# Optimization experiments

Hardware: AMD Instinct MI355X
Metric: run time of the kernel (lower is better)

## Reference

```python
import jax, jax.numpy as jnp
import numpy as np

K = 20          # neighbors, hardcoded in module
SLOPE = 0.2     # LeakyReLU negative slope
EPS = 1e-5      # BatchNorm eps (eval mode, running_mean=0, running_var=1)


def _knn_idx(x, k):
    # x: (B, N, C) -> (B, N, k) indices of k nearest neighbors (includes self)
    xx = jnp.sum(x * x, axis=-1)                      # (B, N)
    inner = jnp.einsum('bnc,bmc->bnm', x, x)          # (B, N, N)
    neg_sqdist = 2.0 * inner - xx[:, :, None] - xx[:, None, :]
    _, idx = jax.lax.top_k(neg_sqdist, k)
    return idx


def _graph_feature(x, k):
    # x: (B, N, C) -> edge features (B, N, k, 2C) = [x_j - x_i, x_i]
    idx = _knn_idx(x, k)
    feat = jax.vmap(lambda xt, ix: xt[ix])(x, idx)    # (B, N, k, C)
    xc = jnp.broadcast_to(x[:, :, None, :], feat.shape)
    return jnp.concatenate([feat - xc, xc], axis=-1)


def _bn_lrelu(h, g, b):
    # eval-mode BN (mean=0, var=1) + LeakyReLU(0.2)
    h = h * (g / jnp.sqrt(1.0 + EPS)) + b
    return jnp.where(h >= 0, h, SLOPE * h)


def _edge_conv(x, W, g, b):
    # EdgeConv block: graph feature -> 1x1 conv -> BN -> LeakyReLU -> max over k
    e = _graph_feature(x, K)                          # (B, N, k, 2C)
    h = jnp.einsum('bnkc,oc->bnko', e, W)
    h = _bn_lrelu(h, g, b)
    return jnp.max(h, axis=2)                         # (B, N, O)


def reference(x, W1, g1, b1, W2, g2, b2, W3, g3, b3, W4, g4, b4, W5, g5, b5, Wemb):
    # x: (B, N, 3) point cloud
    x1 = _edge_conv(x, W1, g1, b1)    # (B, N, 64)
    x2 = _edge_conv(x1, W2, g2, b2)   # (B, N, 64)
    x3 = _edge_conv(x2, W3, g3, b3)   # (B, N, 128)
    x4 = _edge_conv(x3, W4, g4, b4)   # (B, N, 256)
    h = jnp.concatenate([x1, x2, x3, x4], axis=-1)    # (B, N, 512)
    h = jnp.einsum('bnc,oc->bno', h, W5)              # conv5 (1x1)
    h = _bn_lrelu(h, g5, b5)
    h = jnp.max(h, axis=1)                            # global max pool -> (B, 512)
    feat = h[:, None, :]                              # (B, 1, 512)
    embedding = h @ Wemb.T                            # (B, 256)
    return (feat, embedding)


def setup_inputs() -> dict:
    key = jax.random.key(0)
    ks = jax.random.split(key, 18)
    B, N = 8, 2048
    num_features = 256

    def w(k, o, i):
        return jax.random.normal(k, (o, i), dtype=jnp.float32) * (1.0 / np.sqrt(i))

    return {
        'x':  jax.random.normal(ks[0], (B, N, 3), dtype=jnp.float32),
        'W1': w(ks[1], 64, 6),
        'g1': jnp.ones((64,), jnp.float32),  'b1': jnp.zeros((64,), jnp.float32),
        'W2': w(ks[2], 64, 128),
        'g2': jnp.ones((64,), jnp.float32),  'b2': jnp.zeros((64,), jnp.float32),
        'W3': w(ks[3], 128, 128),
        'g3': jnp.ones((128,), jnp.float32), 'b3': jnp.zeros((128,), jnp.float32),
        'W4': w(ks[4], 256, 256),
        'g4': jnp.ones((256,), jnp.float32), 'b4': jnp.zeros((256,), jnp.float32),
        'W5': w(ks[5], 512, 512),
        'g5': jnp.ones((512,), jnp.float32), 'b5': jnp.zeros((512,), jnp.float32),
        'Wemb': w(ks[6], num_features, 512),
    }
```

## Files before the change

### kernel.cpp

```cpp
#include <hip/hip_runtime.h>
#include <hip/hip_bf16.h>

#define BB 8
#define NN 2048
#define KK 20
#define BN (BB*NN)
#define RSQ 0.99999500003749969f

constexpr size_t OFF_XX  = 0;
constexpr size_t OFF_X1  = OFF_XX  + BN;
constexpr size_t OFF_X2  = OFF_X1  + (size_t)BN*64;
constexpr size_t OFF_X3  = OFF_X2  + (size_t)BN*64;
constexpr size_t OFF_X4  = OFF_X3  + (size_t)BN*128;
constexpr size_t OFF_SC  = OFF_X4  + (size_t)BN*256;
constexpr size_t OFF_ID  = OFF_SC  + (size_t)BN*160;
constexpr size_t OFF_W5T = OFF_ID  + (size_t)BN*20;
constexpr size_t OFF_MX  = OFF_W5T + 512*512;
constexpr size_t OFF_MN  = OFF_MX  + BB*512;
constexpr size_t OFF_WT2 = OFF_MN  + BB*512;
constexpr size_t OFF_WT3 = OFF_WT2 + 8192;
constexpr size_t OFF_WT4 = OFF_WT3 + 16384;
constexpr size_t WS_END  = OFF_WT4 + 65536;
constexpr size_t OFF_BIG = WS_END;
constexpr size_t OFF_XCAT = OFF_BIG + (size_t)16*1024*1024;
constexpr size_t WS_BIG_END = OFF_BIG + (size_t)BB*NN*NN;
static_assert(OFF_ID - OFF_X3 >= (size_t)4096*2048, "fallback dual dist fits");
static_assert(OFF_XCAT + (size_t)BN*768 <= WS_BIG_END, "xcat h/m/l fits in dist region");

typedef unsigned short u16;
typedef __attribute__((ext_vector_type(8))) short short8;
typedef __attribute__((ext_vector_type(8))) unsigned short ushort8;
typedef __attribute__((ext_vector_type(4))) float f32x4;

__device__ inline unsigned encf(float f){ unsigned u=__float_as_uint(f); return (u&0x80000000u)? ~u : (u|0x80000000u); }
__device__ inline float decf(unsigned e){ unsigned u=(e&0x80000000u)? (e&0x7fffffffu) : ~e; return __uint_as_float(u); }
__device__ inline float lrelu(float h){ return h>=0.f ? h : 0.2f*h; }
__device__ inline u16 bf16rne(float x){
  unsigned u = __float_as_uint(x);
  return (u16)((u + 0x7FFFu + ((u>>16)&1u)) >> 16);
}
__device__ inline float bf16f(u16 h){ return __uint_as_float((unsigned)h<<16); }
__device__ inline void bf16split3(float v, u16& h, u16& m, u16& l){
  h = bf16rne(v);  float r1 = v  - bf16f(h);
  m = bf16rne(r1); float r2 = r1 - bf16f(m);
  l = bf16rne(r2);
}

__device__ inline float readlane_f(float v, int sl){
  return __int_as_float(__builtin_amdgcn_readlane(__float_as_int(v), sl));
}

#define INSERT_CAND(cv, ci) { \
  unsigned long long mge = __ballot((lv > cv) || (lv == cv && li < ci)); \
  int pos = __popcll(mge); \
  float upv = __shfl_up(lv, 1); \
  int   upi = __shfl_up(li, 1); \
  bool shift = (lane > pos) && (lane < KK); \
  lv = (lane == pos) ? cv : (shift ? upv : lv); \
  li = (lane == pos) ? ci : (shift ? upi : li); \
  theta = readlane_f(lv, KK-1); }

#define BITONIC64_DESC(v, vi) { \
  _Pragma("unroll") \
  for(int k=2; k<=64; k<<=1){ \
    _Pragma("unroll") \
    for(int j=k>>1; j>=1; j>>=1){ \
      float ov = __shfl_xor(v, j); \
      int   oi = __shfl_xor(vi, j); \
      int partner = lane ^ j; \
      bool keepFirst = (((lane & k) == 0)) == (lane < partner); \
      bool before = (v > ov) || (v == ov && vi < oi); \
      if(keepFirst != before){ v = ov; vi = oi; } \
    } \
  } }


__global__ void prep_k(const float* W5, const float* W2, const float* W3, const float* W4,
                       float* W5T, float* WT2, float* WT3, float* WT4,
                       u16* w5h, u16* w5m, u16* w5l,
                       unsigned* mx, unsigned* mn){
  int i = blockIdx.x*256 + threadIdx.x;
  { int o = i>>9, c = i&511; W5T[c*512+o] = W5[i]; }
  {
    int rg = i>>13, kt = (i>>9)&15, l = (i>>3)&63, j = i&7;
    int o = rg*16 + (l&15);
    int c = kt*32 + ((l>>4)<<3) + j;
    u16 h,m,lo; bf16split3(W5[(size_t)o*512 + c], h, m, lo);
    w5h[i]=h; w5m[i]=m; w5l[i]=lo; }
  if(i < 65536){ int c = i>>9, o = i&511;
    WT4[i] = (o<256) ? W4[(size_t)o*256 + c] : W4[(size_t)(o-256)*256 + 128 + c]; }
  if(i < 16384){ int c = i>>8, o = i&255;
    WT3[i] = (o<128) ? W3[(size_t)o*128 + c] : W3[(size_t)(o-128)*128 + 64 + c]; }
  if(i <  8192){ int c = i>>7, o = i&127;
    WT2[i] = (o<64) ? W2[(size_t)o*128 + c] : W2[(size_t)(o-64)*128 + 64 + c]; }
  if(i <  4096){ mx[i] = 0x007FFFFFu; mn[i] = 0xFF800000u; }
}

template<int C>
__launch_bounds__(256) __global__ void sqnorm_k(const float* X, float* xx){
  int i = blockIdx.x*256 + threadIdx.x;
  const float* r = X + (size_t)i*C;
  float s = 0.f;
  #pragma unroll
  for(int c=0;c<C;c++) s = fmaf(r[c], r[c], s);
  xx[i] = s;
}

template<int C>
__launch_bounds__(256) __global__ void split_k(const float* __restrict__ X,
    u16* __restrict__ xh, u16* __restrict__ xm, u16* __restrict__ xl){
  constexpr int KT = C/32;
  const size_t t = (size_t)blockIdx.x*256 + threadIdx.x;
  const int l = (int)(t & 63);
  const size_t tile = t >> 6;
  const int kt = (int)(tile & (KT-1));
  const size_t rgG = tile / KT;
  const size_t row = rgG*16 + (l & 15);
  const int k = kt*32 + ((l>>4)<<3);
  const float* p = X + row*C + k;
  float4 v0 = *(const float4*)p;
  float4 v1 = *(const float4*)(p+4);
  float vs[8] = {v0.x,v0.y,v0.z,v0.w,v1.x,v1.y,v1.z,v1.w};
  ushort8 H,M,L;
  #pragma unroll
  for(int j=0;j<8;j++){ u16 h,m,lo; bf16split3(vs[j],h,m,lo); H[j]=h; M[j]=m; L[j]=lo; }
  *(ushort8*)(xh + t*8) = H;
  *(ushort8*)(xm + t*8) = M;
  *(ushort8*)(xl + t*8) = L;
}

#define FMA_ROW(I) \
  acc[I][0]=fmaf(a,b0v,acc[I][0]); acc[I][1]=fmaf(a,b1v,acc[I][1]); \
  acc[I][2]=fmaf(a,b2v,acc[I][2]); acc[I][3]=fmaf(a,b3v,acc[I][3]); \
  acc[I][4]=fmaf(a,b4v,acc[I][4]); acc[I][5]=fmaf(a,b5v,acc[I][5]); \
  acc[I][6]=fmaf(a,b6v,acc[I][6]); acc[I][7]=fmaf(a,b7v,acc[I][7]);

template<int C>
__launch_bounds__(256) __global__ void gemm_dist_k(const float* __restrict__ X, const float* __restrict__ xx,
                                                   float* __restrict__ dist, int b0){
  constexpr int AST = 188;
  __shared__ __align__(16) float a_sh[16*AST];
  __shared__ __align__(16) float b_sh[16*AST];
  __shared__ float sxn[128], sxm[128];
  const int tid = threadIdx.x;
  const int b   = b0 + blockIdx.z;
  const int mtile = blockIdx.x*128;
  const int ntile = blockIdx.y*128;
  const int tn = tid & 15, tm = tid >> 4;
  const float* Xb  = X  + (size_t)b*NN*C;
  const float* xxb = xx + (size_t)b*NN;
  if(tid < 128) sxn[tid] = xxb[ntile + tid];
  else          sxm[tid-128] = xxb[mtile + tid-128];
  float acc[8][8];
  #pragma unroll
  for(int i=0;i<8;i++){
    #pragma unroll
    for(int j=0;j<8;j++) acc[i][j]=0.f;
  }
  for(int cc=0; cc<C; cc+=16){
    __syncthreads();
    #pragma unroll
    for(int s=0;s<2;s++){
      int ii = tid + 256*s; int r = ii>>2, q = ii&3;
      int pr = r + 4*(r>>3);
      float4 va = *(const float4*)&Xb[(size_t)(ntile + r)*C + cc + 4*q];
      a_sh[(4*q+0)*AST + pr]=va.x; a_sh[(4*q+1)*AST + pr]=va.y;
      a_sh[(4*q+2)*AST + pr]=va.z; a_sh[(4*q+3)*AST + pr]=va.w;
      float4 vb = *(const float4*)&Xb[(size_t)(mtile + r)*C + cc + 4*q];
      b_sh[(4*q+0)*AST + pr]=vb.x; b_sh[(4*q+1)*AST + pr]=vb.y;
      b_sh[(4*q+2)*AST + pr]=vb.z; b_sh[(4*q+3)*AST + pr]=vb.w;
    }
    __syncthreads();
    #pragma unroll
    for(int c=0;c<16;c++){
      float4 A0 = *(const float4*)&a_sh[c*AST + 12*tn];
      float4 A1 = *(const float4*)&a_sh[c*AST + 12*tn + 4];
      float4 B0 = *(const float4*)&b_sh[c*AST + 12*tm];
      float4 B1 = *(const float4*)&b_sh[c*AST + 12*tm + 4];
      float b0v=B0.x,b1v=B0.y,b2v=B0.z,b3v=B0.w,b4v=B1.x,b5v=B1.y,b6v=B1.z,b7v=B1.w;
      float a;
      a=A0.x; FMA_ROW(0)
      a=A0.y; FMA_ROW(1)
      a=A0.z; FMA_ROW(2)
      a=A0.w; FMA_ROW(3)
      a=A1.x; FMA_ROW(4)
      a=A1.y; FMA_ROW(5)
      a=A1.z; FMA_ROW(6)
      a=A1.w; FMA_ROW(7)
    }
  }
  float xnr[8], xmr[8];
  #pragma unroll
  for(int i=0;i<8;i++){ xnr[i]=sxn[tn*8+i]; xmr[i]=sxm[tm*8+i]; }
  const size_t rowb = (size_t)blockIdx.z*NN + ntile + tn*8;
  #pragma unroll
  for(int i=0;i<8;i++){
    float4 w0, w1;
    w0.x=(2.f*acc[i][0]-xnr[i])-xmr[0]; w0.y=(2.f*acc[i][1]-xnr[i])-xmr[1];
    w0.z=(2.f*acc[i][2]-xnr[i])-xmr[2]; w0.w=(2.f*acc[i][3]-xnr[i])-xmr[3];
    w1.x=(2.f*acc[i][4]-xnr[i])-xmr[4]; w1.y=(2.f*acc[i][5]-xnr[i])-xmr[5];
    w1.z=(2.f*acc[i][6]-xnr[i])-xmr[6]; w1.w=(2.f*acc[i][7]-xnr[i])-xmr[7];
    float* dp = dist + (rowb + i)*NN + mtile + tm*8;
    *(float4*)dp = w0;
    *(float4*)(dp+4) = w1;
  }
}

template<int C>
__launch_bounds__(256) __global__ void mfma_dist_k(const u16* __restrict__ xh, const u16* __restrict__ xm,
    const u16* __restrict__ xl, const float* __restrict__ xx, float* __restrict__ dist){
  constexpr int KT = C/32;
  const int tid = threadIdx.x;
  const int l  = tid & 63, wv = tid >> 6;
  const int lg = l >> 4, lr = l & 15;
  const int b  = blockIdx.z;
  const int qrow0 = blockIdx.y*128 + (wv>>1)*64;
  const int crow0 = blockIdx.x*128 + (wv&1)*64;
  const size_t brg = (size_t)b*(NN/16);
  f32x4 acc[4][4];
  #pragma unroll
  for(int m=0;m<4;m++){
    #pragma unroll
    for(int n=0;n<4;n++) acc[m][n] = (f32x4){0.f,0.f,0.f,0.f};
  }
  const size_t abase = (brg + (qrow0>>4))*KT*512 + (size_t)l*8;
  const size_t bbase = (brg + (crow0>>4))*KT*512 + (size_t)l*8;
  for(int kt=0; kt<KT; kt++){
    short8 Ah[4], Am[4], Al[4], Bh[4], Bm[4], Bl[4];
    #pragma unroll
    for(int m=0;m<4;m++){
      size_t o = abase + (size_t)(m*KT + kt)*512;
      Ah[m] = *(const short8*)(xh + o);
      Am[m] = *(const short8*)(xm + o);
      Al[m] = *(const short8*)(xl + o);
    }
    #pragma unroll
    for(int n=0;n<4;n++){
      size_t o = bbase + (size_t)(n*KT + kt)*512;
      Bh[n] = *(const short8*)(xh + o);
      Bm[n] = *(const short8*)(xm + o);
      Bl[n] = *(const short8*)(xl + o);
    }
    #pragma unroll
    for(int m=0;m<4;m++){
      #pragma unroll
      for(int n=0;n<4;n++){
        acc[m][n] = __builtin_amdgcn_mfma_f32_16x16x32_bf16(Ah[m], Bh[n], acc[m][n], 0, 0, 0);
        acc[m][n] = __builtin_amdgcn_mfma_f32_16x16x32_bf16(Ah[m], Bm[n], acc[m][n], 0, 0, 0);
        acc[m][n] = __builtin_amdgcn_mfma_f32_16x16x32_bf16(Am[m], Bh[n], acc[m][n], 0, 0, 0);
        acc[m][n] = __builtin_amdgcn_mfma_f32_16x16x32_bf16(Ah[m], Bl[n], acc[m][n], 0, 0, 0);
        acc[m][n] = __builtin_amdgcn_mfma_f32_16x16x32_bf16(Al[m], Bh[n], acc[m][n], 0, 0, 0);
        acc[m][n] = __builtin_amdgcn_mfma_f32_16x16x32_bf16(Am[m], Bm[n], acc[m][n], 0, 0, 0);
      }
    }
  }
  const float* xxb = xx + (size_t)b*NN;
  float xxc[4];
  #pragma unroll
  for(int n=0;n<4;n++) xxc[n] = xxb[crow0 + n*16 + lr];
  #pragma unroll
  for(int m=0;m<4;m++){
    #pragma unroll
    for(int r=0;r<4;r++){
      int qr = qrow0 + m*16 + 4*lg + r;
      float xq = xxb[qr];
      float* dp = dist + ((size_t)b*NN + qr)*NN + crow0;
      #pragma unroll
      for(int n=0;n<4;n++) dp[n*16 + lr] = (2.f*acc[m][n][r] - xq) - xxc[n];
    }
  }
}

__launch_bounds__(256) __global__ void sel_k(const float* __restrict__ dist, int* __restrict__ id,
                                             int b0, int nrows){
  const int w = (blockIdx.x*256 + threadIdx.x) >> 6;
  const int lane = threadIdx.x & 63;
  if(w >= nrows) return;
  const float* dr = dist + (size_t)w*NN;
  float4 c0 = *(const float4*)&dr[4*lane];
  float cd0[4] = {c0.x, c0.y, c0.z, c0.w};
  int jbest = 0; float v = cd0[0];
  #pragma unroll
  for(int j=1;j<4;j++){ if(cd0[j] > v){ v = cd0[j]; jbest = j; } }
  int vi = 4*lane + jbest;
  BITONIC64_DESC(v, vi)
  float lv = (lane < KK) ? v : -INFINITY;
  int   li = (lane < KK) ? vi : 0;
  float theta = readlane_f(lv, KK-1);
  #pragma unroll
  for(int j=0;j<4;j++){
    float cand = (j == jbest) ? -INFINITY : cd0[j];
    unsigned long long bal = __ballot(cand > theta);
    while(bal){
      int bpos = __ffsll((unsigned long long)bal) - 1;
      bal &= bal - 1;
      float cv = readlane_f(cand, bpos);
      if(cv > theta){
        int ci = 4*bpos + j;
        INSERT_CAND(cv, ci)
      }
    }
  }
  for(int ms=256; ms<NN; ms+=256){
    float4 c4 = *(const float4*)&dr[ms + 4*lane];
    #pragma unroll
    for(int j=0;j<4;j++){
      float cand = (j==0)?c4.x:(j==1)?c4.y:(j==2)?c4.z:c4.w;
      unsigned long long bal = __ballot(cand > theta);
      while(bal){
        int bpos = __ffsll((unsigned long long)bal) - 1;
        bal &= bal - 1;
        float cv = readlane_f(cand, bpos);
        if(cv > theta){
          int ci = ms + 4*bpos + j;
          INSERT_CAND(cv, ci)
        }
      }
    }
  }
  if(lane < KK) id[((size_t)b0*NN + w)*KK + lane] = li;
}

__launch_bounds__(256) __global__ void sel3_k(const float* __restrict__ X, int* __restrict__ id){
  const int gw = (blockIdx.x*256 + threadIdx.x) >> 6;
  const int lane = threadIdx.x & 63;
  const int b = gw >> 11, n = gw & 2047;
  const float* Xb  = X + (size_t)b*NN*3;
  const float x0v = Xb[n*3], x1v = Xb[n*3+1], x2v = Xb[n*3+2];
  float xxn = 0.f;
  xxn = fmaf(x0v, x0v, xxn); xxn = fmaf(x1v, x1v, xxn); xxn = fmaf(x2v, x2v, xxn);
  float lv, theta; int li;
  {
    const float* p = Xb + (size_t)(4*lane)*3;
    float4 va = *(const float4*)p;
    float4 vb = *(const float4*)(p+4);
    float4 vc = *(const float4*)(p+8);
    float cx[4] = {va.x, va.w, vb.z, vc.y};
    float cy[4] = {va.y, vb.x, vb.w, vc.z};
    float cz[4] = {va.z, vb.y, vc.x, vc.w};
    float cd[4];
    #pragma unroll
    for(int j=0;j<4;j++){
      float s = 0.f;
      s = fmaf(x0v, cx[j], s); s = fmaf(x1v, cy[j], s); s = fmaf(x2v, cz[j], s);
      float xxm = 0.f;
      xxm = fmaf(cx[j], cx[j], xxm); xxm = fmaf(cy[j], cy[j], xxm); xxm = fmaf(cz[j], cz[j], xxm);
      cd[j] = (2.f*s - xxn) - xxm;
    }
    int jbest = 0; float v = cd[0];
    #pragma unroll
    for(int j=1;j<4;j++){ if(cd[j] > v){ v = cd[j]; jbest = j; } }
    int vi = 4*lane + jbest;
    BITONIC64_DESC(v, vi)
    lv = (lane < KK) ? v : -INFINITY;
    li = (lane < KK) ? vi : 0;
    theta = readlane_f(lv, KK-1);
    #pragma unroll
    for(int j=0;j<4;j++){
      float cand = (j == jbest) ? -INFINITY : cd[j];
      unsigned long long bal = __ballot(cand > theta);
      while(bal){
        int bpos = __ffsll((unsigned long long)bal) - 1;
        bal &= bal - 1;
        float cv = readlane_f(cand, bpos);
        if(cv > theta){
          int ci = 4*bpos + j;
          INSERT_CAND(cv, ci)
        }
      }
    }
  }
  for(int ms=256; ms<NN; ms+=256){
    const float* p = Xb + (size_t)(ms + 4*lane)*3;
    float4 va = *(const float4*)p;
    float4 vb = *(const float4*)(p+4);
    float4 vc = *(const float4*)(p+8);
    float cx[4] = {va.x, va.w, vb.z, vc.y};
    float cy[4] = {va.y, vb.x, vb.w, vc.z};
    float cz[4] = {va.z, vb.y, vc.x, vc.w};
    float cd[4];
    #pragma unroll
    for(int j=0;j<4;j++){
      float s = 0.f;
      s = fmaf(x0v, cx[j], s); s = fmaf(x1v, cy[j], s); s = fmaf(x2v, cz[j], s);
      float xxm = 0.f;
      xxm = fmaf(cx[j], cx[j], xxm); xxm = fmaf(cy[j], cy[j], xxm); xxm = fmaf(cz[j], cz[j], xxm);
      cd[j] = (2.f*s - xxn) - xxm;
    }
    #pragma unroll
    for(int j=0;j<4;j++){
      float cand = cd[j];
      unsigned long long bal = __ballot(cand > theta);
      while(bal){
        int bpos = __ffsll((unsigned long long)bal) - 1;
        bal &= bal - 1;
        float cv = readlane_f(cand, bpos);
        if(cv > theta){
          int ci = ms + 4*bpos + j;
          INSERT_CAND(cv, ci)
        }
      }
    }
  }
  if(lane < KK) id[(size_t)gw*KK + lane] = li;
}

__launch_bounds__(256) __global__ void qp3_k(const float* X, const float* W, float* qp){
  const int t   = blockIdx.x*256 + threadIdx.x;
  const int row = t >> 3;
  const int c0  = (t & 7) * 8;
  float xn[3];
  #pragma unroll
  for(int c=0;c<3;c++) xn[c] = X[(size_t)row*3 + c];
  for(int oi=c0; oi<c0+8; oi++){
    const float* w = W + (size_t)oi*6;
    float aq=0.f, ap=0.f;
    #pragma unroll
    for(int c=0;c<3;c++){ aq = fmaf(xn[c], w[c], aq); ap = fmaf(xn[c], w[3+c], ap); }
    qp[(size_t)row*128 + oi]      = aq;
    qp[(size_t)row*128 + 64 + oi] = ap;
  }
}

template<int CIN, int W2C>
__launch_bounds__(256) __global__ void qp_gemm_k(const float* __restrict__ X, const float* __restrict__ WT,
                                                 float* __restrict__ qp){
  constexpr int ASTA = 92;
  constexpr int ASTB = 188;
  __shared__ __align__(16) float a_sh[16*ASTA];
  __shared__ __align__(16) float b_sh[16*ASTB];
  const int tid = threadIdx.x;
  const int otile = blockIdx.x*128;
  const int rtile = blockIdx.y*64;
  const int tn = tid & 15, tm = tid >> 4;
  const int aoff = 4*tn + 4*(tn>>1);
  float acc[4][8];
  #pragma unroll
  for(int i=0;i<4;i++){
    #pragma unroll
    for(int j=0;j<8;j++) acc[i][j]=0.f;
  }
  for(int cc=0; cc<CIN; cc+=16){
    __syncthreads();
    { int r = tid>>2, q = tid&3;
      int pr = r + 4*(r>>3);
      float4 va = *(const float4*)&X[(size_t)(rtile + r)*CIN + cc + 4*q];
      a_sh[(4*q+0)*ASTA + pr]=va.x; a_sh[(4*q+1)*ASTA + pr]=va.y;
      a_sh[(4*q+2)*ASTA + pr]=va.z; a_sh[(4*q+3)*ASTA + pr]=va.w; }
    #pragma unroll
    for(int s=0;s<2;s++){
      int ii = tid + 256*s;
      int cl = ii>>5, o4 = ii&31;
      float4 vb = *(const float4*)&WT[(size_t)(cc+cl)*W2C + otile + 4*o4];
      *(float4*)&b_sh[cl*ASTB + 4*o4 + 4*(o4>>1)] = vb;
    }
    __syncthreads();
    #pragma unroll
    for(int c=0;c<16;c++){
      float4 A0 = *(const float4*)&a_sh[c*ASTA + aoff];
      float4 B0 = *(const float4*)&b_sh[c*ASTB + 12*tm];
      float4 B1 = *(const float4*)&b_sh[c*ASTB + 12*tm + 4];
      float b0v=B0.x,b1v=B0.y,b2v=B0.z,b3v=B0.w,b4v=B1.x,b5v=B1.y,b6v=B1.z,b7v=B1.w;
      float a;
      a=A0.x; FMA_ROW(0)
      a=A0.y; FMA_ROW(1)
      a=A0.z; FMA_ROW(2)
      a=A0.w; FMA_ROW(3)
    }
  }
  #pragma unroll
  for(int i=0;i<4;i++){
    float* dp = qp + (size_t)(rtile + tn*4 + i)*W2C + otile + tm*8;
    *(float4*)dp     = make_float4(acc[i][0],acc[i][1],acc[i][2],acc[i][3]);
    *(float4*)(dp+4) = make_float4(acc[i][4],acc[i][5],acc[i][6],acc[i][7]);
  }
}

template<int COUT>
__launch_bounds__(256) __global__ void gather_qp_k(const float* __restrict__ qp, const int* __restrict__ idx,
    const float* g, const float* bb, float* out){
  const int t  = blockIdx.x*256 + threadIdx.x;
  const int o  = t % COUT;
  const int bn = t / COUT;
  const int b  = bn >> 11;
  const int* id = idx + (size_t)bn*KK;
  float qv = qp[(size_t)bn*(2*COUT) + o];
  float pv = qp[(size_t)bn*(2*COUT) + COUT + o];
  float base = pv - qv;
  float mx = -INFINITY, mn = INFINITY;
  #pragma unroll
  for(int k=0;k<KK;k++){
    int ik = id[k];
    float v = qp[((size_t)((b<<11) + ik))*(2*COUT) + o];
    mx = fmaxf(mx, v); mn = fminf(mn, v);
  }
  float a  = g[o] * RSQ;
  float bo = bb[o];
  out[(size_t)bn*COUT + o] = lrelu((a >= 0.f ? a*(mx+base) : a*(mn+base)) + bo);
}

template<int CIN, int COUT>
__launch_bounds__(256) __global__ void qp64T_k(const float* __restrict__ X, const float* __restrict__ WT,
                                               int cb, float* __restrict__ q, float* __restrict__ bs){
  const int t   = blockIdx.x*256 + threadIdx.x;
  const int row = t >> 3;
  const int o0  = cb + (t & 7) * 8;
  float xn[CIN];
  #pragma unroll
  for(int c=0;c<CIN;c+=4){ float4 v = *(const float4*)(X + (size_t)row*CIN + c);
    xn[c]=v.x; xn[c+1]=v.y; xn[c+2]=v.z; xn[c+3]=v.w; }
  float aq[8], ap[8];
  #pragma unroll
  for(int j=0;j<8;j++){ aq[j]=0.f; ap[j]=0.f; }
  #pragma unroll 4
  for(int c=0;c<CIN;c++){
    float xc = xn[c];
    float4 wa0 = *(const float4*)&WT[(size_t)c*(2*COUT) + o0];
    float4 wa1 = *(const float4*)&WT[(size_t)c*(2*COUT) + o0 + 4];
    float4 wb0 = *(const float4*)&WT[(size_t)c*(2*COUT) + COUT + o0];
    float4 wb1 = *(const float4*)&WT[(size_t)c*(2*COUT) + COUT + o0 + 4];
    aq[0]=fmaf(xc,wa0.x,aq[0]); aq[1]=fmaf(xc,wa0.y,aq[1]); aq[2]=fmaf(xc,wa0.z,aq[2]); aq[3]=fmaf(xc,wa0.w,aq[3]);
    aq[4]=fmaf(xc,wa1.x,aq[4]); aq[5]=fmaf(xc,wa1.y,aq[5]); aq[6]=fmaf(xc,wa1.z,aq[6]); aq[7]=fmaf(xc,wa1.w,aq[7]);
    ap[0]=fmaf(xc,wb0.x,ap[0]); ap[1]=fmaf(xc,wb0.y,ap[1]); ap[2]=fmaf(xc,wb0.z,ap[2]); ap[3]=fmaf(xc,wb0.w,ap[3]);
    ap[4]=fmaf(xc,wb1.x,ap[4]); ap[5]=fmaf(xc,wb1.y,ap[5]); ap[6]=fmaf(xc,wb1.z,ap[6]); ap[7]=fmaf(xc,wb1.w,ap[7]);
  }
  float* qpp = q  + (size_t)row*64 + (o0-cb);
  float* bpp = bs + (size_t)row*64 + (o0-cb);
  *(float4*)qpp     = make_float4(aq[0],aq[1],aq[2],aq[3]);
  *(float4*)(qpp+4) = make_float4(aq[4],aq[5],aq[6],aq[7]);
  *(float4*)bpp     = make_float4(ap[0]-aq[0],ap[1]-aq[1],ap[2]-aq[2],ap[3]-aq[3]);
  *(float4*)(bpp+4) = make_float4(ap[4]-aq[4],ap[5]-aq[5],ap[6]-aq[6],ap[7]-aq[7]);
}

template<int CFULL>
__launch_bounds__(256) __global__ void gather_chunk_k(const float* q, const float* bs, const int* idx,
    const float* g, const float* bb, int cb, float* out){
  const int t  = blockIdx.x*256 + threadIdx.x;
  const int o  = t & 63;
  const int bn = t >> 6;
  const int b  = bn >> 11;
  const int* id = idx + (size_t)bn*KK;
  float base = bs[t];
  float mx = -INFINITY, mn = INFINITY;
  #pragma unroll
  for(int k=0;k<KK;k++){
    int ik = id[k];
    float v = q[((size_t)((b<<11) + ik))*64 + o];
    mx = fmaxf(mx, v); mn = fminf(mn, v);
  }
  float a  = g[cb+o] * RSQ;
  float bo = bb[cb+o];
  out[(size_t)bn*CFULL + cb + o] = lrelu((a >= 0.f ? a*(mx+base) : a*(mn+base)) + bo);
}

__launch_bounds__(256) __global__ void w5gemm_k(const float* __restrict__ x1, const float* __restrict__ x2,
    const float* __restrict__ x3, const float* __restrict__ x4,
    const float* __restrict__ W5T, unsigned* mxe, unsigned* mne){
  constexpr int ASTA = 92;
  constexpr int ASTB = 188;
  __shared__ __align__(16) float a_sh[16*ASTA];
  __shared__ __align__(16) float b_sh[16*ASTB];
  const int tid = threadIdx.x;
  const int otile = blockIdx.x*128;
  const int rtile = blockIdx.y*64;
  const int b     = blockIdx.z;
  const int tn = tid & 15, tm = tid >> 4;
  const int aoff = 4*tn + 4*(tn>>1);
  const size_t row0 = (size_t)b*NN + rtile;
  float acc[4][8];
  #pragma unroll
  for(int i=0;i<4;i++){
    #pragma unroll
    for(int j=0;j<8;j++) acc[i][j]=0.f;
  }
  for(int cc=0; cc<512; cc+=16){
    const float* src; int stride, coff;
    if(cc<64)      { src=x1; stride=64;  coff=cc; }
    else if(cc<128){ src=x2; stride=64;  coff=cc-64; }
    else if(cc<256){ src=x3; stride=128; coff=cc-128; }
    else           { src=x4; stride=256; coff=cc-256; }
    __syncthreads();
    { int r = tid>>2, q = tid&3;
      int pr = r + 4*(r>>3);
      float4 va = *(const float4*)&src[(row0 + r)*stride + coff + 4*q];
      a_sh[(4*q+0)*ASTA + pr]=va.x; a_sh[(4*q+1)*ASTA + pr]=va.y;
      a_sh[(4*q+2)*ASTA + pr]=va.z; a_sh[(4*q+3)*ASTA + pr]=va.w; }
    #pragma unroll
    for(int s=0;s<2;s++){
      int ii = tid + 256*s;
      int cl = ii>>5, o4 = ii&31;
      float4 vb = *(const float4*)&W5T[(size_t)(cc+cl)*512 + otile + 4*o4];
      *(float4*)&b_sh[cl*ASTB + 4*o4 + 4*(o4>>1)] = vb;
    }
    __syncthreads();
    #pragma unroll
    for(int c=0;c<16;c++){
      float4 A0 = *(const float4*)&a_sh[c*ASTA + aoff];
      float4 B0 = *(const float4*)&b_sh[c*ASTB + 12*tm];
      float4 B1 = *(const float4*)&b_sh[c*ASTB + 12*tm + 4];
      float b0v=B0.x,b1v=B0.y,b2v=B0.z,b3v=B0.w,b4v=B1.x,b5v=B1.y,b6v=B1.z,b7v=B1.w;
      float a;
      a=A0.x; FMA_ROW(0)
      a=A0.y; FMA_ROW(1)
      a=A0.z; FMA_ROW(2)
      a=A0.w; FMA_ROW(3)
    }
  }
  #pragma unroll
  for(int j=0;j<8;j++){
    float M=-INFINITY, m=INFINITY;
    #pragma unroll
    for(int i=0;i<4;i++){ M=fmaxf(M,acc[i][j]); m=fminf(m,acc[i][j]); }
    #pragma unroll
    for(int d=1; d<16; d<<=1){
      M = fmaxf(M, __shfl_xor(M, d));
      m = fminf(m, __shfl_xor(m, d));
    }
    if(tn == 0){
      int o = otile + tm*8 + j;
      atomicMax(&mxe[b*512+o], encf(M));
      atomicMin(&mne[b*512+o], encf(m));
    }
  }
}

__launch_bounds__(256) __global__ void cvt_k(const float* __restrict__ x1, const float* __restrict__ x2,
    const float* __restrict__ x3, const float* __restrict__ x4,
    u16* __restrict__ xh, u16* __restrict__ xm, u16* __restrict__ xl){
  const size_t t = (size_t)blockIdx.x*256 + threadIdx.x;
  const int l = (int)(t & 63);
  const size_t tile = t >> 6;
  const int kt = (int)(tile & 15);
  const size_t rgG = tile >> 4;
  const size_t row = rgG*16 + (l & 15);
  const int col = kt*32 + ((l>>4)<<3);
  const float* src; int stride, coff;
  if(col<64)      { src=x1; stride=64;  coff=col; }
  else if(col<128){ src=x2; stride=64;  coff=col-64; }
  else if(col<256){ src=x3; stride=128; coff=col-128; }
  else            { src=x4; stride=256; coff=col-256; }
  const float* p = src + row*stride + coff;
  float4 v0 = *(const float4*)p;
  float4 v1 = *(const float4*)(p+4);
  float vs[8] = {v0.x,v0.y,v0.z,v0.w,v1.x,v1.y,v1.z,v1.w};
  ushort8 H, M, L;
  #pragma unroll
  for(int j=0;j<8;j++){ u16 h,m,lo; bf16split3(vs[j],h,m,lo); H[j]=h; M[j]=m; L[j]=lo; }
  *(ushort8*)(xh + t*8) = H;
  *(ushort8*)(xm + t*8) = M;
  *(ushort8*)(xl + t*8) = L;
}

__launch_bounds__(256) __global__ void w5mfma_k(const u16* __restrict__ xh, const u16* __restrict__ xm,
    const u16* __restrict__ xl,
    const u16* __restrict__ wh, const u16* __restrict__ wm, const u16* __restrict__ wl,
    unsigned* mxe, unsigned* mne){
  const int tid = threadIdx.x;
  const int l  = tid & 63, wv = tid >> 6;
  const int lg = l >> 4, lr = l & 15;
  const int row0 = blockIdx.y*128 + (wv>>1)*64;
  const int col0 = blockIdx.x*128 + (wv&1)*64;
  const int b = blockIdx.y >> 4;
  f32x4 acc[4][4];
  #pragma unroll
  for(int m=0;m<4;m++){
    #pragma unroll
    for(int n=0;n<4;n++) acc[m][n] = (f32x4){0.f,0.f,0.f,0.f};
  }
  const size_t abase = (size_t)(row0>>4)*16*512 + (size_t)l*8;
  const size_t bbase = (size_t)(col0>>4)*16*512 + (size_t)l*8;
  for(int kt=0; kt<16; kt++){
    short8 Ah[4], Am[4], Al[4], Bh[4], Bm[4], Bl[4];
    #pragma unroll
    for(int m=0;m<4;m++){
      size_t o = abase + (size_t)(m*16 + kt)*512;
      Ah[m] = *(const short8*)(xh + o);
      Am[m] = *(const short8*)(xm + o);
      Al[m] = *(const short8*)(xl + o);
    }
    #pragma unroll
    for(int n=0;n<4;n++){
      size_t o = bbase + (size_t)(n*16 + kt)*512;
      Bh[n] = *(const short8*)(wh + o);
      Bm[n] = *(const short8*)(wm + o);
      Bl[n] = *(const short8*)(wl + o);
    }
    #pragma unroll
    for(int m=0;m<4;m++){
      #pragma unroll
      for(int n=0;n<4;n++){
        acc[m][n] = __builtin_amdgcn_mfma_f32_16x16x32_bf16(Ah[m], Bh[n], acc[m][n], 0, 0, 0);
        acc[m][n] = __builtin_amdgcn_mfma_f32_16x16x32_bf16(Ah[m], Bm[n], acc[m][n], 0, 0, 0);
        acc[m][n] = __builtin_amdgcn_mfma_f32_16x16x32_bf16(Am[m], Bh[n], acc[m][n], 0, 0, 0);
        acc[m][n] = __builtin_amdgcn_mfma_f32_16x16x32_bf16(Ah[m], Bl[n], acc[m][n], 0, 0, 0);
        acc[m][n] = __builtin_amdgcn_mfma_f32_16x16x32_bf16(Al[m], Bh[n], acc[m][n], 0, 0, 0);
        acc[m][n] = __builtin_amdgcn_mfma_f32_16x16x32_bf16(Am[m], Bm[n], acc[m][n], 0, 0, 0);
      }
    }
  }
  #pragma unroll
  for(int n=0;n<4;n++){
    float M = -INFINITY, mnv = INFINITY;
    #pragma unroll
    for(int m=0;m<4;m++){
      #pragma unroll
      for(int r=0;r<4;r++){ float v = acc[m][n][r]; M = fmaxf(M, v); mnv = fminf(mnv, v); }
    }
    M   = fmaxf(M,   __shfl_xor(M, 16));   M   = fmaxf(M,   __shfl_xor(M, 32));
    mnv = fminf(mnv, __shfl_xor(mnv, 16)); mnv = fminf(mnv, __shfl_xor(mnv, 32));
    if(lg == 0){
      int o = col0 + n*16 + lr;
      atomicMax(&mxe[b*512+o], encf(M));
      atomicMin(&mne[b*512+o], encf(mnv));
    }
  }
}

__launch_bounds__(256) __global__ void final_k(const unsigned* mxe, const unsigned* mne,
    const float* g5, const float* b5, const float* Wemb, float* out){
  const int b = blockIdx.x, t = threadIdx.x;
  __shared__ float h[512];
  for(int o=t; o<512; o+=256){
    float mx = decf(mxe[b*512+o]);
    float mn = decf(mne[b*512+o]);
    float a  = g5[o] * RSQ;
    float bo = b5[o];
    float hv = lrelu((a >= 0.f ? a*mx : a*mn) + bo);
    h[o] = hv;
    out[b*512+o] = hv;
  }
  __syncthreads();
  const float* wr = Wemb + (size_t)t*512;
  float s = 0.f;
  for(int o=0;o<512;o+=4){
    float4 w4 = *(const float4*)(wr+o);
    s = fmaf(h[o],w4.x, fmaf(h[o+1],w4.y, fmaf(h[o+2],w4.z, fmaf(h[o+3],w4.w, s))));
  }
  out[4096 + b*256 + t] = s;
}

extern "C" void kernel_launch(void* const* d_in, const int* in_sizes, int n_in,
                              void* d_out, int out_size, void* d_ws, size_t ws_size,
                              hipStream_t stream) {
  if (ws_size < WS_END * sizeof(float)) return;
  const bool big = ws_size >= WS_BIG_END * sizeof(float);

  const float* x0   = (const float*)d_in[0];
  const float* W1   = (const float*)d_in[1];
  const float* g1   = (const float*)d_in[2];
  const float* b1   = (const float*)d_in[3];
  const float* W2   = (const float*)d_in[4];
  const float* g2   = (const float*)d_in[5];
  const float* b2   = (const float*)d_in[6];
  const float* W3   = (const float*)d_in[7];
  const float* g3   = (const float*)d_in[8];
  const float* b3   = (const float*)d_in[9];
  const float* W4   = (const float*)d_in[10];
  const float* g4   = (const float*)d_in[11];
  const float* b4   = (const float*)d_in[12];
  const float* W5   = (const float*)d_in[13];
  const float* g5   = (const float*)d_in[14];
  const float* b5   = (const float*)d_in[15];
  const float* Wemb = (const float*)d_in[16];

  float* ws = (float*)d_ws;
  float* xx = ws + OFF_XX;
  float* x1 = ws + OFF_X1;  float* x2 = ws + OFF_X2;
  float* x3 = ws + OFF_X3;  float* x4 = ws + OFF_X4;
  float* qpS = ws + OFF_SC;
  float* bsS = ws + OFF_SC + (size_t)BN*64;
  int*   id = (int*)(ws + OFF_ID);
  float* W5Tf = ws + OFF_W5T;
  unsigned* mxe = (unsigned*)(ws + OFF_MX);
  unsigned* mne = (unsigned*)(ws + OFF_MN);
  float* WT2 = ws + OFF_WT2;
  float* WT3 = ws + OFF_WT3;
  float* WT4 = ws + OFF_WT4;
  float* distD = ws + OFF_X3;
  float* distS = ws + OFF_X4;
  float* distB = ws + OFF_BIG;
  u16* w5h = (u16*)(ws + OFF_SC + (size_t)BN*128);
  u16* w5m = w5h + 512*512;
  u16* w5l = w5m + 512*512;
  float* out = (float*)d_out;

  prep_k<<<1024,256,0,stream>>>(W5, W2, W3, W4, W5Tf, WT2, WT3, WT4, w5h, w5m, w5l, mxe, mne);

  sel3_k<<<BN*64/256,256,0,stream>>>(x0, id);
  qp3_k<<<BN*8/256,256,0,stream>>>(x0, W1, qpS);
  gather_qp_k<64><<<BN*64/256,256,0,stream>>>(qpS, id, g1, b1, x1);

  if(big){
    float* qpB = distB;
    u16* sh = (u16*)x4;
    { u16* sm = sh + (size_t)BN*64; u16* sl = sm + (size_t)BN*64;
      sqnorm_k<64><<<BN/256,256,0,stream>>>(x1, xx);
      split_k<64><<<BN*64/8/256,256,0,stream>>>(x1, sh, sm, sl);
      mfma_dist_k<64><<<dim3(16,16,8),256,0,stream>>>(sh, sm, sl, xx, distB);
      sel_k<<<(8*NN)/4,256,0,stream>>>(distB, id, 0, 8*NN);
      qp_gemm_k<64,128><<<dim3(1,BN/64),256,0,stream>>>(x1, WT2, qpB);
      gather_qp_k<64><<<BN*64/256,256,0,stream>>>(qpB, id, g2, b2, x2); }
    { u16* sm = sh + (size_t)BN*64; u16* sl = sm + (size_t)BN*64;
      sqnorm_k<64><<<BN/256,256,0,stream>>>(x2, xx);
      split_k<64><<<BN*64/8/256,256,0,stream>>>(x2, sh, sm, sl);
      mfma_dist_k<64><<<dim3(16,16,8),256,0,stream>>>(sh, sm, sl, xx, distB);
      sel_k<<<(8*NN)/4,256,0,stream>>>(distB, id, 0, 8*NN);
      qp_gemm_k<64,256><<<dim3(2,BN/64),256,0,stream>>>(x2, WT3, qpB);
      gather_qp_k<128><<<BN*128/256,256,0,stream>>>(qpB, id, g3, b3, x3); }
    { u16* sm = sh + (size_t)BN*128; u16* sl = sm + (size_t)BN*128;
      sqnorm_k<128><<<BN/256,256,0,stream>>>(x3, xx);
      split_k<128><<<BN*128/8/256,256,0,stream>>>(x3, sh, sm, sl);
      mfma_dist_k<128><<<dim3(16,16,8),256,0,stream>>>(sh, sm, sl, xx, distB);
      sel_k<<<(8*NN)/4,256,0,stream>>>(distB, id, 0, 8*NN);
      qp_gemm_k<128,512><<<dim3(4,BN/64),256,0,stream>>>(x3, WT4, qpB);
      gather_qp_k<256><<<BN*256/256,256,0,stream>>>(qpB, id, g4, b4, x4); }
    u16* xh = (u16*)(ws + OFF_XCAT);
    u16* xm = xh + (size_t)BN*512;
    u16* xl = xm + (size_t)BN*512;
    cvt_k<<<BN*512/8/256,256,0,stream>>>(x1, x2, x3, x4, xh, xm, xl);
    w5mfma_k<<<dim3(4,128),256,0,stream>>>(xh, xm, xl, w5h, w5m, w5l, mxe, mne);
  } else {
    sqnorm_k<64><<<BN/256,256,0,stream>>>(x1, xx);
    for(int r=0;r<4;r++){
      gemm_dist_k<64><<<dim3(16,16,2),256,0,stream>>>(x1, xx, distD, 2*r);
      sel_k<<<(2*NN)/4,256,0,stream>>>(distD, id, 2*r, 2*NN);
    }
    qp64T_k<64,64><<<BN*8/256,256,0,stream>>>(x1, WT2, 0, qpS, bsS);
    gather_chunk_k<64><<<BN*64/256,256,0,stream>>>(qpS, bsS, id, g2, b2, 0, x2);

    sqnorm_k<64><<<BN/256,256,0,stream>>>(x2, xx);
    for(int r=0;r<4;r++){
      gemm_dist_k<64><<<dim3(16,16,2),256,0,stream>>>(x2, xx, distD, 2*r);
      sel_k<<<(2*NN)/4,256,0,stream>>>(distD, id, 2*r, 2*NN);
    }
    for(int cb=0; cb<128; cb+=64){
      qp64T_k<64,128><<<BN*8/256,256,0,stream>>>(x2, WT3, cb, qpS, bsS);
      gather_chunk_k<128><<<BN*64/256,256,0,stream>>>(qpS, bsS, id, g3, b3, cb, x3);
    }

    sqnorm_k<128><<<BN/256,256,0,stream>>>(x3, xx);
    for(int r=0;r<8;r++){
      gemm_dist_k<128><<<dim3(16,16,1),256,0,stream>>>(x3, xx, distS, r);
      sel_k<<<NN/4,256,0,stream>>>(distS, id, r, NN);
    }
    for(int cb=0; cb<256; cb+=64){
      qp64T_k<128,256><<<BN*8/256,256,0,stream>>>(x3, WT4, cb, qpS, bsS);
      gather_chunk_k<256><<<BN*64/256,256,0,stream>>>(qpS, bsS, id, g4, b4, cb, x4);
    }
    w5gemm_k<<<dim3(4,32,8),256,0,stream>>>(x1, x2, x3, x4, W5Tf, mxe, mne);
  }

  final_k<<<BB,256,0,stream>>>(mxe, mne, g5, b5, Wemb, out);
}
```

Baseline: 617.9 us.

## Chunk distance/select per four batches and use split-bf16 MFMA for layer-4 projection

Distance computation and top-k selection now run in two chunks of four batches each. This lets the 4-batch dist matrix stay smaller and more cache-resident between the write and the select read. The layer-4 q/p projection GEMM is replaced by an MFMA kernel using a 3-way bf16 split of the activations, reusing the already-split x3, and of pre-split W4 weights, emulating fp32 accuracy with six MFMAs per tile. The W5 transpose is skipped on the big path, and its buffer is reused for the split weights. This adds kernel launches and depends on the bf16x3 split being accurate enough for downstream top-k.

```diff
diff --git a/kernel.cpp b/kernel.cpp
--- a/kernel.cpp
+++ b/kernel.cpp
@@ -32,6 +32,10 @@
 typedef __attribute__((ext_vector_type(8))) unsigned short ushort8;
 typedef __attribute__((ext_vector_type(4))) float f32x4;
 
+constexpr size_t WTS_2H = 0,      WTS_2M = 8192,   WTS_2L = 16384;
+constexpr size_t WTS_3H = 24576,  WTS_3M = 40960,  WTS_3L = 57344;
+constexpr size_t WTS_4H = 73728,  WTS_4M = 139264, WTS_4L = 204800;
+
 __device__ inline unsigned encf(float f){ unsigned u=__float_as_uint(f); return (u&0x80000000u)? ~u : (u|0x80000000u); }
 __device__ inline float decf(unsigned e){ unsigned u=(e&0x80000000u)? (e&0x7fffffffu) : ~e; return __uint_as_float(u); }
 __device__ inline float lrelu(float h){ return h>=0.f ? h : 0.2f*h; }
@@ -77,10 +81,10 @@
 
 __global__ void prep_k(const float* W5, const float* W2, const float* W3, const float* W4,
                        float* W5T, float* WT2, float* WT3, float* WT4,
-                       u16* w5h, u16* w5m, u16* w5l,
-                       unsigned* mx, unsigned* mn){
+                       u16* w5h, u16* w5m, u16* w5l, u16* wts,
+                       unsigned* mx, unsigned* mn, int big){
   int i = blockIdx.x*256 + threadIdx.x;
-  { int o = i>>9, c = i&511; W5T[c*512+o] = W5[i]; }
+  if(!big){ int o = i>>9, c = i&511; W5T[c*512+o] = W5[i]; }
   {
     int rg = i>>13, kt = (i>>9)&15, l = (i>>3)&63, j = i&7;
     int o = rg*16 + (l&15);
@@ -93,6 +97,15 @@
     WT3[i] = (o<128) ? W3[(size_t)o*128 + c] : W3[(size_t)(o-128)*128 + 64 + c]; }
   if(i <  8192){ int c = i>>7, o = i&127;
     WT2[i] = (o<64) ? W2[(size_t)o*128 + c] : W2[(size_t)(o-64)*128 + 64 + c]; }
+  if(big){
+    if(i < 65536){
+      int rg=i>>11, kt=(i>>9)&3, l=(i>>3)&63, j=i&7;
+      int o = rg*16 + (l&15);
+      int c = kt*32 + ((l>>4)<<3) + j;
+      float v = (o<256) ? W4[(size_t)o*256 + c] : W4[(size_t)(o-256)*256 + 128 + c];
+      u16 h,m,lo; bf16split3(v,h,m,lo);
+      wts[WTS_4H+i]=h; wts[WTS_4M+i]=m; wts[WTS_4L+i]=lo; }
+  }
   if(i <  4096){ mx[i] = 0x007FFFFFu; mn[i] = 0xFF800000u; }
 }
 
@@ -208,12 +221,13 @@
 
 template<int C>
 __launch_bounds__(256) __global__ void mfma_dist_k(const u16* __restrict__ xh, const u16* __restrict__ xm,
-    const u16* __restrict__ xl, const float* __restrict__ xx, float* __restrict__ dist){
+    const u16* __restrict__ xl, const float* __restrict__ xx, float* __restrict__ dist, int b0){
   constexpr int KT = C/32;
   const int tid = threadIdx.x;
   const int l  = tid & 63, wv = tid >> 6;
   const int lg = l >> 4, lr = l & 15;
-  const int b  = blockIdx.z;
+  const int cz = blockIdx.z;
+  const int b  = b0 + cz;
   const int qrow0 = blockIdx.y*128 + (wv>>1)*64;
   const int crow0 = blockIdx.x*128 + (wv&1)*64;
   const size_t brg = (size_t)b*(NN/16);
@@ -264,7 +278,7 @@
     for(int r=0;r<4;r++){
       int qr = qrow0 + m*16 + 4*lg + r;
       float xq = xxb[qr];
-      float* dp = dist + ((size_t)b*NN + qr)*NN + crow0;
+      float* dp = dist + ((size_t)cz*NN + qr)*NN + crow0;
       #pragma unroll
       for(int n=0;n<4;n++) dp[n*16 + lr] = (2.f*acc[m][n][r] - xq) - xxc[n];
     }
@@ -473,6 +487,65 @@
     float* dp = qp + (size_t)(rtile + tn*4 + i)*W2C + otile + tm*8;
     *(float4*)dp     = make_float4(acc[i][0],acc[i][1],acc[i][2],acc[i][3]);
     *(float4*)(dp+4) = make_float4(acc[i][4],acc[i][5],acc[i][6],acc[i][7]);
+  }
+}
+
+__launch_bounds__(256) __global__ void qp_mfma4_k(const u16* __restrict__ xh, const u16* __restrict__ xm,
+    const u16* __restrict__ xl,
+    const u16* __restrict__ wh, const u16* __restrict__ wm, const u16* __restrict__ wl,
+    float* __restrict__ qp){
+  constexpr int KT = 4;
+  const int tid = threadIdx.x;
+  const int l  = tid & 63, wv = tid >> 6;
+  const int lg = l >> 4, lr = l & 15;
+  const int row0 = blockIdx.y*128 + (wv>>1)*64;
+  const int col0 = blockIdx.x*128 + (wv&1)*64;
+  f32x4 acc[4][4];
+  #pragma unroll
+  for(int m=0;m<4;m++){
+    #pragma unroll
+    for(int n=0;n<4;n++) acc[m][n] = (f32x4){0.f,0.f,0.f,0.f};
+  }
+  const size_t abase = (size_t)(row0>>4)*KT*512 + (size_t)l*8;
+  const size_t bbase = (size_t)(col0>>4)*KT*512 + (size_t)l*8;
+  for(int kt=0; kt<KT; kt++){
+    short8 Ah[4], Am[4], Al[4], Bh[4], Bm[4], Bl[4];
+    #pragma unroll
+    for(int m=0;m<4;m++){
+      size_t o = abase + (size_t)(m*KT + kt)*512;
+      Ah[m] = *(const short8*)(xh + o);
+      Am[m] = *(const short8*)(xm + o);
+      Al[m] = *(const short8*)(xl + o);
+    }
+    #pragma unroll
+    for(int n=0;n<4;n++){
+      size_t o = bbase + (size_t)(n*KT + kt)*512;
+      Bh[n] = *(const short8*)(wh + o);
+      Bm[n] = *(const short8*)(wm + o);
+      Bl[n] = *(const short8*)(wl + o);
+    }
+    #pragma unroll
+    for(int m=0;m<4;m++){
+      #pragma unroll
+      for(int n=0;n<4;n++){
+        acc[m][n] = __builtin_amdgcn_mfma_f32_16x16x32_bf16(Ah[m], Bh[n], acc[m][n], 0, 0, 0);
+        acc[m][n] = __builtin_amdgcn_mfma_f32_16x16x32_bf16(Ah[m], Bm[n], acc[m][n], 0, 0, 0);
+        acc[m][n] = __builtin_amdgcn_mfma_f32_16x16x32_bf16(Am[m], Bh[n], acc[m][n], 0, 0, 0);
+        acc[m][n] = __builtin_amdgcn_mfma_f32_16x16x32_bf16(Ah[m], Bl[n], acc[m][n], 0, 0, 0);
+        acc[m][n] = __builtin_amdgcn_mfma_f32_16x16x32_bf16(Al[m], Bh[n], acc[m][n], 0, 0, 0);
+        acc[m][n] = __builtin_amdgcn_mfma_f32_16x16x32_bf16(Am[m], Bm[n], acc[m][n], 0, 0, 0);
+      }
+    }
+  }
+  #pragma unroll
+  for(int m=0;m<4;m++){
+    #pragma unroll
+    for(int r=0;r<4;r++){
+      int row = row0 + m*16 + 4*lg + r;
+      float* dp = qp + (size_t)row*512 + col0;
+      #pragma unroll
+      for(int n=0;n<4;n++) dp[n*16 + lr] = acc[m][n][r];
+    }
   }
 }
 
@@ -782,9 +855,11 @@
   u16* w5h = (u16*)(ws + OFF_SC + (size_t)BN*128);
   u16* w5m = w5h + 512*512;
   u16* w5l = w5m + 512*512;
+  u16* wts = (u16*)W5Tf;
   float* out = (float*)d_out;
 
-  prep_k<<<1024,256,0,stream>>>(W5, W2, W3, W4, W5Tf, WT2, WT3, WT4, w5h, w5m, w5l, mxe, mne);
+  prep_k<<<1024,256,0,stream>>>(W5, W2, W3, W4, W5Tf, WT2, WT3, WT4,
+                                w5h, w5m, w5l, wts, mxe, mne, big ? 1 : 0);
 
   sel3_k<<<BN*64/256,256,0,stream>>>(x0, id);
   qp3_k<<<BN*8/256,256,0,stream>>>(x0, W1, qpS);
@@ -796,23 +871,30 @@
     { u16* sm = sh + (size_t)BN*64; u16* sl = sm + (size_t)BN*64;
       sqnorm_k<64><<<BN/256,256,0,stream>>>(x1, xx);
       split_k<64><<<BN*64/8/256,256,0,stream>>>(x1, sh, sm, sl);
-      mfma_dist_k<64><<<dim3(16,16,8),256,0,stream>>>(sh, sm, sl, xx, distB);
-      sel_k<<<(8*NN)/4,256,0,stream>>>(distB, id, 0, 8*NN);
+      for(int c0=0;c0<BB;c0+=4){
+        mfma_dist_k<64><<<dim3(16,16,4),256,0,stream>>>(sh, sm, sl, xx, distB, c0);
+        sel_k<<<(4*NN)/4,256,0,stream>>>(distB, id, c0, 4*NN);
+      }
       qp_gemm_k<64,128><<<dim3(1,BN/64),256,0,stream>>>(x1, WT2, qpB);
       gather_qp_k<64><<<BN*64/256,256,0,stream>>>(qpB, id, g2, b2, x2); }
     { u16* sm = sh + (size_t)BN*64; u16* sl = sm + (size_t)BN*64;
       sqnorm_k<64><<<BN/256,256,0,stream>>>(x2, xx);
       split_k<64><<<BN*64/8/256,256,0,stream>>>(x2, sh, sm, sl);
-      mfma_dist_k<64><<<dim3(16,16,8),256,0,stream>>>(sh, sm, sl, xx, distB);
-      sel_k<<<(8*NN)/4,256,0,stream>>>(distB, id, 0, 8*NN);
+      for(int c0=0;c0<BB;c0+=4){
+        mfma_dist_k<64><<<dim3(16,16,4),256,0,stream>>>(sh, sm, sl, xx, distB, c0);
+        sel_k<<<(4*NN)/4,256,0,stream>>>(distB, id, c0, 4*NN);
+      }
       qp_gemm_k<64,256><<<dim3(2,BN/64),256,0,stream>>>(x2, WT3, qpB);
       gather_qp_k<128><<<BN*128/256,256,0,stream>>>(qpB, id, g3, b3, x3); }
     { u16* sm = sh + (size_t)BN*128; u16* sl = sm + (size_t)BN*128;
       sqnorm_k<128><<<BN/256,256,0,stream>>>(x3, xx);
       split_k<128><<<BN*128/8/256,256,0,stream>>>(x3, sh, sm, sl);
-      mfma_dist_k<128><<<dim3(16,16,8),256,0,stream>>>(sh, sm, sl, xx, distB);
-      sel_k<<<(8*NN)/4,256,0,stream>>>(distB, id, 0, 8*NN);
-      qp_gemm_k<128,512><<<dim3(4,BN/64),256,0,stream>>>(x3, WT4, qpB);
+      for(int c0=0;c0<BB;c0+=4){
+        mfma_dist_k<128><<<dim3(16,16,4),256,0,stream>>>(sh, sm, sl, xx, distB, c0);
+        sel_k<<<(4*NN)/4,256,0,stream>>>(distB, id, c0, 4*NN);
+      }
+      qp_mfma4_k<<<dim3(4,BN/128),256,0,stream>>>(sh, sm, sl,
+          wts+WTS_4H, wts+WTS_4M, wts+WTS_4L, qpB);
       gather_qp_k<256><<<BN*256/256,256,0,stream>>>(qpB, id, g4, b4, x4); }
     u16* xh = (u16*)(ws + OFF_XCAT);
     u16* xm = xh + (size_t)BN*512;
```

Result: faster. 600.8 us (-2.8%).
